# Kernel optimization log

Hardware: AMD Instinct MI355X
Metric: run time of the kernel (lower is better)

## Reference

```python
import jax, jax.numpy as jnp
import numpy as np
import math

D_MODEL = 1024
N_HEADS = 16
D_HEAD = D_MODEL // N_HEADS
NUM_BUCKETS = 32
MAX_DISTANCE = 128
B, LQ, LK = 2, 2048, 2048


def _rel_pos_bucket(rel):
    # rel: [Lq, Lk] int32, rel = mem - ctx
    n = jnp.clip(-rel, 0, None)
    max_exact = NUM_BUCKETS // 2
    is_small = n < max_exact
    val_if_large = max_exact + (
        jnp.log(n.astype(jnp.float32) / max_exact + 1e-9)
        / math.log(MAX_DISTANCE / max_exact)
        * (NUM_BUCKETS - max_exact)
    ).astype(jnp.int32)
    val_if_large = jnp.minimum(val_if_large, NUM_BUCKETS - 1)
    return jnp.where(is_small, n, val_if_large)


def setup_inputs() -> dict:
    key = jax.random.key(0)
    ks = jax.random.split(key, 9)
    scale = 1.0 / math.sqrt(D_MODEL)
    q = jax.random.normal(ks[0], (B, LQ, D_MODEL), dtype=jnp.float32)
    k = jax.random.normal(ks[1], (B, LK, D_MODEL), dtype=jnp.float32)
    v = jax.random.normal(ks[2], (B, LK, D_MODEL), dtype=jnp.float32)
    key_padding_mask = jax.random.randint(ks[3], (B, 1, 1, LK), 0, 2).astype(bool)
    Wq = jax.random.normal(ks[4], (D_MODEL, D_MODEL), dtype=jnp.float32) * scale
    Wk = jax.random.normal(ks[5], (D_MODEL, D_MODEL), dtype=jnp.float32) * scale
    Wv = jax.random.normal(ks[6], (D_MODEL, D_MODEL), dtype=jnp.float32) * scale
    Wo = jax.random.normal(ks[7], (D_MODEL, D_MODEL), dtype=jnp.float32) * scale
    rel_emb = jax.random.normal(ks[8], (NUM_BUCKETS, N_HEADS), dtype=jnp.float32) * 0.02
    return {"q": q, "k": k, "v": v, "key_padding_mask": key_padding_mask,
            "Wq": Wq, "Wk": Wk, "Wv": Wv, "Wo": Wo, "rel_emb": rel_emb}


def reference(q, k, v, key_padding_mask, Wq, Wk, Wv, Wo, rel_emb):
    Bq, Lq, _ = q.shape
    Lk = k.shape[1]
    # projections (nn.Linear: x @ W.T), split heads -> [B, H, L, dh]
    qh = (q @ Wq.T).reshape(Bq, Lq, N_HEADS, D_HEAD).transpose(0, 2, 1, 3)
    kh = (k @ Wk.T).reshape(Bq, Lk, N_HEADS, D_HEAD).transpose(0, 2, 1, 3)
    vh = (v @ Wv.T).reshape(Bq, Lk, N_HEADS, D_HEAD).transpose(0, 2, 1, 3)
    scores = jnp.einsum('bhqd,bhkd->bhqk', qh, kh) / math.sqrt(D_HEAD)
    # relative position bias: [1, H, Lq, Lk]
    rel = jnp.arange(Lk, dtype=jnp.int32)[None, :] - jnp.arange(Lq, dtype=jnp.int32)[:, None]
    buckets = _rel_pos_bucket(rel)  # [Lq, Lk]
    bias = rel_emb[buckets]         # [Lq, Lk, H]
    scores = scores + bias.transpose(2, 0, 1)[None]
    scores = jnp.where(key_padding_mask, scores, -1e9)
    attn = jax.nn.softmax(scores, axis=-1)
    out = jnp.einsum('bhqk,bhkd->bhqd', attn, vh)
    out = out.transpose(0, 2, 1, 3).reshape(Bq, Lq, D_MODEL)
    return out @ Wo.T
```

## Files before the change

kernel.cpp:

```cpp
#include <hip/hip_runtime.h>
#include <math.h>

typedef _Float16 f16;
typedef __fp16 h16x2 __attribute__((ext_vector_type(2)));
typedef _Float16 f16x4 __attribute__((ext_vector_type(4)));
typedef _Float16 f16x8 __attribute__((ext_vector_type(8)));
typedef float f32x4 __attribute__((ext_vector_type(4)));
typedef float f32x16 __attribute__((ext_vector_type(16)));
typedef unsigned int u32;

#define D_MODEL 1024
#define NHEADS 16
#define DHEAD 64
#define LQ 2048
#define LKK 2048
#define BB 2
#define LOG2E 1.4426950408889634f

static __device__ __forceinline__ void gload16(const void* g, void* l) {
  __builtin_amdgcn_global_load_lds(
      (const __attribute__((address_space(1))) u32*)g,
      (__attribute__((address_space(3))) u32*)l, 16, 0, 0);
}
static __device__ __forceinline__ float ex2(float x) {
  float r;
  asm volatile("v_exp_f32 %0, %1\n\ts_nop 0" : "=v"(r) : "v"(x));
  return r;
}
static __device__ __forceinline__ u32 pkr(float a, float b) {
  union { h16x2 h; u32 u; } c;
  c.h = __builtin_amdgcn_cvt_pkrtz(a, b);
  return c.u;
}
static __device__ __forceinline__ float fmax3(float a, float b, float c) {
  return fmaxf(fmaxf(a, b), c);
}
#define MFMA16(a, b, c) __builtin_amdgcn_mfma_f32_16x16x32_f16(a, b, c, 0, 0, 0)
#define MFMA32(a, b, c) __builtin_amdgcn_mfma_f32_32x32x16_f16(a, b, c, 0, 0, 0)

__global__ void k_cvtw_prep(const float* Wq, const float* Wk, const float* Wv, const float* Wo,
                            f16* W16, const void* msk, const float* __restrict__ rel,
                            float* __restrict__ biasT, unsigned char* __restrict__ m8) {
  const int blk = blockIdx.x;
  const int t = threadIdx.x;
  if (blk < 4096) {
    int i = blk * 256 + t;
    int which = i >> 18, off = i & 262143;
    const float* s = which == 0 ? Wq : (which == 1 ? Wk : (which == 2 ? Wv : Wo));
    float4 x = ((const float4*)s)[off];
    f16x4 o; o[0] = (f16)x.x; o[1] = (f16)x.y; o[2] = (f16)x.z; o[3] = (f16)x.w;
    ((f16x4*)(W16 + (size_t)which * 1048576))[off] = o;
    return;
  }
  if (blk == 4096) {
    __shared__ int o1s, o2s;
    if (t == 0) { o1s = 0; o2s = 0; }
    __syncthreads();
    const unsigned char* raw = (const unsigned char*)msk;
    int o1 = 0, o2 = 0;
    for (int i = t; i < BB * LKK; i += 256) {
      unsigned char vv = raw[i];
      if ((i & 3) && vv) o1 = 1;
      if (((i & 3) == 2) && vv == 0x80u) o2 = 1;
    }
    if (o1) atomicOr(&o1s, 1);
    if (o2) atomicOr(&o2s, 1);
    __syncthreads();
    const int f = o1s ? (o2s ? 2 : 1) : 0;
    for (int i = t; i < BB * LKK; i += 256) {
      unsigned char v;
      if (f == 0)      v = (((const int*)msk)[i] != 0);
      else if (f == 1) v = (((const unsigned char*)msk)[i] != 0);
      else             v = (((const float*)msk)[i] != 0.0f);
      m8[i] = v;
    }
    return;
  }
  for (int n = t; n < 2048; n += 256) {
    int bucket;
    if (n < 16) bucket = n;
    else {
      float tt = logf((float)n / 16.0f + 1e-9f);
      tt = tt / 2.0794415416798357f;
      tt = tt * 16.0f;
      bucket = 16 + (int)tt;
      if (bucket > 31) bucket = 31;
    }
    for (int h = 0; h < NHEADS; ++h)
      biasT[h * 2048 + n] = rel[bucket * NHEADS + h] * LOG2E;
  }
}

template <int EPI, int BN, bool AF32>
static __device__ __forceinline__ void gemm_core(const void* __restrict__ Av,
                                                 const f16* __restrict__ Bm,
                                                 void* __restrict__ C) {
  constexpr int JN = BN / 32;
  __shared__ __align__(16) f16 sA[128 * 32];
  __shared__ __align__(16) f16 sB[BN * 32];
  const int t = threadIdx.x;
  const int w = t >> 6, lane = t & 63;
  const int lg = lane >> 4, lc = lane & 15;
  const int wr = w >> 1, wc = w & 1;
  const long row0 = (long)blockIdx.x * 128;
  const long col0 = (long)blockIdx.y * BN;
  f32x4 acc[4][JN] = {};

  for (int kk = 0; kk < 1024; kk += 32) {
#pragma unroll
    for (int it = 0; it < 2; ++it) {
      int ch = t + it * 256;
      int r = ch >> 2, kq = ch & 3;
      if constexpr (AF32) {
        const float* src = (const float*)Av + (row0 + r) * 1024 + kk + kq * 8;
        float4 x0 = *(const float4*)src;
        float4 x1 = *(const float4*)(src + 4);
        f16x8 o;
        o[0] = (f16)x0.x; o[1] = (f16)x0.y; o[2] = (f16)x0.z; o[3] = (f16)x0.w;
        o[4] = (f16)x1.x; o[5] = (f16)x1.y; o[6] = (f16)x1.z; o[7] = (f16)x1.w;
        *(f16x8*)((char*)sA + ch * 16) = o;
      } else {
        gload16((const f16*)Av + (row0 + r) * 1024 + kk + kq * 8, (char*)sA + ch * 16);
      }
    }
#pragma unroll
    for (int it = 0; it < BN / 64; ++it) {
      int ch = t + it * 256;
      int r = ch >> 2, kq = ch & 3;
      gload16(Bm + (col0 + r) * 1024 + kk + kq * 8, (char*)sB + ch * 16);
    }
    __syncthreads();
    f16x8 af[4], bf[JN];
#pragma unroll
    for (int i = 0; i < 4; ++i)
      af[i] = *(const f16x8*)&sA[(wr * 64 + i * 16 + lc) * 32 + lg * 8];
#pragma unroll
    for (int j = 0; j < JN; ++j)
      bf[j] = *(const f16x8*)&sB[(wc * (16 * JN) + j * 16 + lc) * 32 + lg * 8];
#pragma unroll
    for (int i = 0; i < 4; ++i)
#pragma unroll
      for (int j = 0; j < JN; ++j)
        acc[i][j] = MFMA16(af[i], bf[j], acc[i][j]);
    __syncthreads();
  }
#pragma unroll
  for (int i = 0; i < 4; ++i)
#pragma unroll
    for (int j = 0; j < JN; ++j) {
      const long rowb = row0 + wr * 64 + i * 16 + lg * 4;
      const long col = col0 + wc * (16 * JN) + j * 16 + lc;
      if (EPI == 2) {
        long b = rowb >> 11, l0 = rowb & 2047;
        long h = col >> 6, d = col & 63;
        f16x4 ov;
#pragma unroll
        for (int r = 0; r < 4; ++r) ov[r] = (f16)acc[i][j][r];
        *(f16x4*)((f16*)C + (((b * NHEADS + h) * DHEAD + d) * (long)LKK + l0)) = ov;
      } else {
#pragma unroll
        for (int r = 0; r < 4; ++r) {
          long row = rowb + r;
          float v = acc[i][j][r];
          if (EPI == 0) {
            long b = row >> 11, l = row & 2047;
            long h = col >> 6, d = col & 63;
            ((f16*)C)[(((b * NHEADS + h) * LQ) + l) * DHEAD + d] = (f16)v;
          } else {
            ((float*)C)[row * 1024 + col] = v;
          }
        }
      }
    }
}

__global__ void __launch_bounds__(256, 3)
k_gemm_qkv(const float* __restrict__ q, const float* __restrict__ k, const float* __restrict__ v,
           const f16* __restrict__ W16, f16* __restrict__ QHp, f16* __restrict__ KHp,
           f16* __restrict__ VTp) {
  const int z = blockIdx.z;
  if (z == 2) {
    gemm_core<2, 128, true>(v, W16 + 2 * 1048576, VTp);
  } else {
    const float* A = z == 0 ? q : k;
    f16* C = z == 0 ? QHp : KHp;
    gemm_core<0, 128, true>(A, W16 + (size_t)z * 1048576, C);
  }
}

__global__ void __launch_bounds__(256, 2)
k_gemm_o(const f16* __restrict__ A, const f16* __restrict__ Bm, float* __restrict__ C) {
  gemm_core<1, 64, false>(A, Bm, C);
}

__global__ void __launch_bounds__(256, 2)
k_attn(const f16* __restrict__ QH, const f16* __restrict__ KH, const f16* __restrict__ VT,
       const float* __restrict__ BIASg, const unsigned char* __restrict__ M8,
       f16* __restrict__ O16) {
  __shared__ __align__(16) f16 sK[2][64 * 64];
  __shared__ __align__(16) f16 sVT[2][64 * 64];
  __shared__ __align__(16) float sBias[4104];
  __shared__ __align__(16) float sPen[2048];

  const int L = blockIdx.x;
  const int bh = (L & 7) * 4 + ((L >> 3) & 3);
  const int qc = L >> 5;
  const int b = bh >> 4, h = bh & 15;
  const int t = threadIdx.x, w = t >> 6, lane = t & 63;
  const int lq = lane & 31;
  const int hi = lane >> 5;
  const int q0w = qc * 128 + w * 32;
  const size_t base = (size_t)bh * LKK * DHEAD;

  for (int i = t; i < 4104; i += 256) {
    int n = i - 2052; n = n < 0 ? 0 : (n > 2047 ? 2047 : n);
    sBias[i] = BIASg[h * 2048 + n];
  }
  for (int i = t; i < 2048; i += 256)
    sPen[i] = M8[b * LKK + i] ? 0.0f : -3.0e9f;

  f16x8 qb[4];
  const f16* qrow = QH + base + (size_t)(q0w + lq) * DHEAD;
#pragma unroll
  for (int s = 0; s < 4; ++s)
    qb[s] = *(const f16x8*)(qrow + s * 16 + hi * 8);

  const int ch0 = t, ch1 = t + 256;
  const int r0 = ch0 >> 3, g0 = ((ch0 & 7) ^ (r0 & 7)) * 8;
  const int r1 = ch1 >> 3, g1 = ((ch1 & 7) ^ (r1 & 7)) * 8;
  const f16* Kb = KH + base;
  const f16* Vb = VT + base;

  auto STAGE_K = [&](int kt, int buf) {
    const int k0 = kt * 64;
    gload16(Kb + (size_t)(k0 + r0) * DHEAD + g0, (char*)&sK[buf][0] + ch0 * 16);
    gload16(Kb + (size_t)(k0 + r1) * DHEAD + g1, (char*)&sK[buf][0] + ch1 * 16);
  };
  auto STAGE_V = [&](int kt, int buf) {
    const int k0 = kt * 64;
    gload16(Vb + (size_t)r0 * LKK + k0 + g0, (char*)&sVT[buf][0] + ch0 * 16);
    gload16(Vb + (size_t)r1 * LKK + k0 + g1, (char*)&sVT[buf][0] + ch1 * 16);
  };

  float m_r = -1e30f;
  f32x16 oacc0 = {}, oacc1 = {}, oaccL = {};
  const float c1 = 0.125f * LOG2E;
  f16x8 ones;
#pragma unroll
  for (int e = 0; e < 8; ++e) ones[e] = (f16)1.0f;

  auto QK = [&](int kt, f32x16& sa0, f32x16& sa1) {
    const char* sKb = (const char*)&sK[kt & 1][0];
    __builtin_amdgcn_s_setprio(1);
#pragma unroll
    for (int s = 0; s < 4; ++s) {
      f16x8 k0 = *(const f16x8*)(sKb + ((lq * 128 + s * 32 + hi * 16) ^ ((lq & 7) << 4)));
      f16x8 k1 = *(const f16x8*)(sKb + (((32 + lq) * 128 + s * 32 + hi * 16) ^ ((lq & 7) << 4)));
      sa0 = MFMA32(k0, qb[s], sa0);
      sa1 = MFMA32(k1, qb[s], sa1);
    }
    __builtin_amdgcn_s_setprio(0);
  };

  auto SOFTPV = [&](int kt, f32x16& sa0, f32x16& sa1) {
    float p_[32];
#pragma unroll
    for (int r = 0; r < 16; ++r) { p_[r] = sa0[r]; p_[16 + r] = sa1[r]; }

#pragma unroll
    for (int u = 0; u < 8; ++u) {
      int tt = u >> 2, j = u & 3;
      int kbase = kt * 64 + tt * 32 + j * 8 + hi * 4;
      f32x4 pen4 = *(const f32x4*)&sPen[kbase];
      int bidx0 = (q0w + lq) - kbase + 2052;
#pragma unroll
      for (int e = 0; e < 4; ++e) {
        float bp = sBias[bidx0 - e] + pen4[e];
        int r = tt * 16 + j * 4 + e;
        p_[r] = p_[r] * c1 + bp;
      }
    }

    float mm[11];
#pragma unroll
    for (int r = 0; r < 10; ++r) mm[r] = fmax3(p_[3 * r], p_[3 * r + 1], p_[3 * r + 2]);
    mm[10] = fmaxf(p_[30], p_[31]);
    float a0 = fmax3(mm[0], mm[1], mm[2]);
    float a1 = fmax3(mm[3], mm[4], mm[5]);
    float a2 = fmax3(mm[6], mm[7], mm[8]);
    float a3 = fmax3(mm[9], mm[10], a0);
    float mx = fmax3(a1, a2, a3);
    mx = fmaxf(mx, __shfl_xor(mx, 32));

    if (__any(mx > m_r + 8.0f)) {
      float mnew = fmaxf(m_r, mx);
      float al = ex2(m_r - mnew);
      m_r = mnew;
#pragma unroll
      for (int r = 0; r < 16; ++r) { oacc0[r] *= al; oacc1[r] *= al; oaccL[r] *= al; }
    }

#pragma unroll
    for (int r = 0; r < 32; ++r) p_[r] = ex2(p_[r] - m_r);

    f16x8 pf[4];
#pragma unroll
    for (int sl = 0; sl < 4; ++sl) {
      int tt = sl >> 1, sp = sl & 1;
      int bA = tt * 16 + (2 * sp) * 4, bB = tt * 16 + (2 * sp + 1) * 4;
      u32 A0 = pkr(p_[bA], p_[bA + 1]);
      u32 A1 = pkr(p_[bA + 2], p_[bA + 3]);
      u32 B0 = pkr(p_[bB], p_[bB + 1]);
      u32 B1 = pkr(p_[bB + 2], p_[bB + 3]);
      asm volatile("v_permlane32_swap_b32 %0, %1" : "+v"(A0), "+v"(B0));
      asm volatile("v_permlane32_swap_b32 %0, %1" : "+v"(A1), "+v"(B1));
      union { u32 u[4]; f16x8 v; } c;
      c.u[0] = A0; c.u[1] = A1; c.u[2] = B0; c.u[3] = B1;
      pf[sl] = c.v;
    }

    const char* sVb = (const char*)&sVT[kt & 1][0];
    __builtin_amdgcn_s_setprio(1);
#pragma unroll
    for (int sl = 0; sl < 4; ++sl) {
      int K0 = sl * 16;
      f16x8 v0 = *(const f16x8*)(sVb + ((lq * 128 + K0 * 2 + hi * 16) ^ ((lq & 7) << 4)));
      f16x8 v1 = *(const f16x8*)(sVb + (((32 + lq) * 128 + K0 * 2 + hi * 16) ^ ((lq & 7) << 4)));
      oacc0 = MFMA32(v0, pf[sl], oacc0);
      oacc1 = MFMA32(v1, pf[sl], oacc1);
      oaccL = MFMA32(ones, pf[sl], oaccL);
    }
    __builtin_amdgcn_s_setprio(0);
  };

  STAGE_K(0, 0);
  STAGE_V(0, 0);
  STAGE_K(1, 1);
  __syncthreads();
  f32x16 sA0 = {}, sA1 = {}, sB0 = {}, sB1 = {};
  QK(0, sA0, sA1);

  for (int kt = 0; kt < 32; kt += 2) {
    if (kt + 2 < 32) STAGE_K(kt + 2, 0);
    STAGE_V(kt + 1, 1);
    sB0 = f32x16{}; sB1 = f32x16{};
    QK(kt + 1, sB0, sB1);
    SOFTPV(kt, sA0, sA1);
    __syncthreads();
    if (kt + 3 < 32) STAGE_K(kt + 3, 1);
    if (kt + 2 < 32) {
      STAGE_V(kt + 2, 0);
      sA0 = f32x16{}; sA1 = f32x16{};
      QK(kt + 2, sA0, sA1);
    }
    SOFTPV(kt + 1, sB0, sB1);
    __syncthreads();
  }

  const float rinv = 1.0f / oaccL[0];
  const size_t orow = ((size_t)b * LQ + (q0w + lq)) * D_MODEL + h * DHEAD;
#pragma unroll
  for (int dh = 0; dh < 2; ++dh)
#pragma unroll
    for (int j = 0; j < 4; ++j) {
      int d0 = dh * 32 + j * 8 + hi * 4;
      f16x4 ov;
#pragma unroll
      for (int e = 0; e < 4; ++e) {
        float x = (dh ? oacc1[j * 4 + e] : oacc0[j * 4 + e]) * rinv;
        ov[e] = (f16)x;
      }
      *(f16x4*)(O16 + orow + d0) = ov;
    }
}

extern "C" void kernel_launch(void* const* d_in, const int* in_sizes, int n_in,
                              void* d_out, int out_size, void* d_ws, size_t ws_size,
                              hipStream_t stream) {
  (void)in_sizes; (void)n_in; (void)out_size; (void)ws_size;
  const float* q   = (const float*)d_in[0];
  const float* k   = (const float*)d_in[1];
  const float* v   = (const float*)d_in[2];
  const void*  msk = d_in[3];
  const float* Wq  = (const float*)d_in[4];
  const float* Wk  = (const float*)d_in[5];
  const float* Wv  = (const float*)d_in[6];
  const float* Wo  = (const float*)d_in[7];
  const float* rel = (const float*)d_in[8];

  char* ws = (char*)d_ws;
  const size_t SL = (size_t)8 << 20;
  f16* QHp = (f16*)(ws + 0 * SL);
  f16* KHp = (f16*)(ws + 1 * SL);
  f16* VTp = (f16*)(ws + 2 * SL);
  f16* O16 = (f16*)(ws + 3 * SL);
  f16* W16 = (f16*)(ws + 4 * SL);
  char* misc = ws + 5 * SL;
  float* BIAS = (float*)misc;
  unsigned char* M8 = (unsigned char*)(misc + (192 << 10));

  k_cvtw_prep<<<4098, 256, 0, stream>>>(Wq, Wk, Wv, Wo, W16, msk, rel, BIAS, M8);
  k_gemm_qkv<<<dim3(32, 8, 3), 256, 0, stream>>>(q, k, v, W16, QHp, KHp, VTp);
  k_attn<<<512, 256, 0, stream>>>(QHp, KHp, VTp, BIAS, M8, O16);
  k_gemm_o<<<dim3(32, 16), 256, 0, stream>>>(O16, W16 + 3 * 1048576, (float*)d_out);
}
```

Before: 140.8 us.

## Split attention over key halves, read K/V directly, double-buffer GEMM tiles

The attention kernel can now split the key range in two (split-KV): it writes partial normalized outputs plus running max and sum, and a new combine kernel merges the two halves. K and V are read straight from global memory instead of being staged through double-buffered LDS. The bias table now covers only the window this query block needs. The shared GEMM core gains LDS double buffering with register prefetch of the fp32 A tile, and launch bounds are raised to 4 blocks per CU. More blocks and occupancy come at the cost of an extra kernel, extra global traffic for the partials, and uncoalesced direct K/V loads.

After: 238.5 us. +69.4%, slower.

```diff
diff --git a/kernel.cpp b/kernel.cpp
--- a/kernel.cpp
+++ b/kernel.cpp
@@ -96,8 +96,8 @@
                                                  const f16* __restrict__ Bm,
                                                  void* __restrict__ C) {
   constexpr int JN = BN / 32;
-  __shared__ __align__(16) f16 sA[128 * 32];
-  __shared__ __align__(16) f16 sB[BN * 32];
+  __shared__ __align__(16) f16 sA[2][128 * 32];
+  __shared__ __align__(16) f16 sB[2][BN * 32];
   const int t = threadIdx.x;
   const int w = t >> 6, lane = t & 63;
   const int lg = lane >> 4, lc = lane & 15;
@@ -106,44 +106,71 @@
   const long col0 = (long)blockIdx.y * BN;
   f32x4 acc[4][JN] = {};
 
-  for (int kk = 0; kk < 1024; kk += 32) {
-#pragma unroll
-    for (int it = 0; it < 2; ++it) {
-      int ch = t + it * 256;
-      int r = ch >> 2, kq = ch & 3;
-      if constexpr (AF32) {
-        const float* src = (const float*)Av + (row0 + r) * 1024 + kk + kq * 8;
-        float4 x0 = *(const float4*)src;
-        float4 x1 = *(const float4*)(src + 4);
-        f16x8 o;
-        o[0] = (f16)x0.x; o[1] = (f16)x0.y; o[2] = (f16)x0.z; o[3] = (f16)x0.w;
-        o[4] = (f16)x1.x; o[5] = (f16)x1.y; o[6] = (f16)x1.z; o[7] = (f16)x1.w;
-        *(f16x8*)((char*)sA + ch * 16) = o;
-      } else {
-        gload16((const f16*)Av + (row0 + r) * 1024 + kk + kq * 8, (char*)sA + ch * 16);
-      }
-    }
+  const int rA0 = t >> 2, kA0 = t & 3;
+  const int rA1 = (t + 256) >> 2, kA1 = t & 3;
+
+  float4 a[4];
+
+  auto LOADA = [&](int kk) {
+    const float* s0 = (const float*)Av + (row0 + rA0) * 1024 + kk * 32 + kA0 * 8;
+    const float* s1 = (const float*)Av + (row0 + rA1) * 1024 + kk * 32 + kA1 * 8;
+    a[0] = *(const float4*)s0; a[1] = *(const float4*)(s0 + 4);
+    a[2] = *(const float4*)s1; a[3] = *(const float4*)(s1 + 4);
+  };
+  auto WRITEA = [&](int buf) {
+    f16x8 o0, o1;
+    o0[0] = (f16)a[0].x; o0[1] = (f16)a[0].y; o0[2] = (f16)a[0].z; o0[3] = (f16)a[0].w;
+    o0[4] = (f16)a[1].x; o0[5] = (f16)a[1].y; o0[6] = (f16)a[1].z; o0[7] = (f16)a[1].w;
+    o1[0] = (f16)a[2].x; o1[1] = (f16)a[2].y; o1[2] = (f16)a[2].z; o1[3] = (f16)a[2].w;
+    o1[4] = (f16)a[3].x; o1[5] = (f16)a[3].y; o1[6] = (f16)a[3].z; o1[7] = (f16)a[3].w;
+    *(f16x8*)((char*)&sA[buf][0] + t * 16) = o0;
+    *(f16x8*)((char*)&sA[buf][0] + (t + 256) * 16) = o1;
+  };
+  auto STAGEA16 = [&](int kk, int buf) {
+    gload16((const f16*)Av + (row0 + rA0) * 1024 + kk * 32 + kA0 * 8,
+            (char*)&sA[buf][0] + t * 16);
+    gload16((const f16*)Av + (row0 + rA1) * 1024 + kk * 32 + kA1 * 8,
+            (char*)&sA[buf][0] + (t + 256) * 16);
+  };
+  auto STAGEB = [&](int kk, int buf) {
 #pragma unroll
     for (int it = 0; it < BN / 64; ++it) {
       int ch = t + it * 256;
       int r = ch >> 2, kq = ch & 3;
-      gload16(Bm + (col0 + r) * 1024 + kk + kq * 8, (char*)sB + ch * 16);
-    }
-    __syncthreads();
+      gload16(Bm + (col0 + r) * 1024 + kk * 32 + kq * 8, (char*)&sB[buf][0] + ch * 16);
+    }
+  };
+  auto COMPUTE = [&](int buf) {
     f16x8 af[4], bf[JN];
 #pragma unroll
     for (int i = 0; i < 4; ++i)
-      af[i] = *(const f16x8*)&sA[(wr * 64 + i * 16 + lc) * 32 + lg * 8];
+      af[i] = *(const f16x8*)&sA[buf][(wr * 64 + i * 16 + lc) * 32 + lg * 8];
 #pragma unroll
     for (int j = 0; j < JN; ++j)
-      bf[j] = *(const f16x8*)&sB[(wc * (16 * JN) + j * 16 + lc) * 32 + lg * 8];
+      bf[j] = *(const f16x8*)&sB[buf][(wc * (16 * JN) + j * 16 + lc) * 32 + lg * 8];
 #pragma unroll
     for (int i = 0; i < 4; ++i)
 #pragma unroll
       for (int j = 0; j < JN; ++j)
         acc[i][j] = MFMA16(af[i], bf[j], acc[i][j]);
+  };
+
+  if constexpr (AF32) { LOADA(0); } else { STAGEA16(0, 0); }
+  STAGEB(0, 0);
+  if constexpr (AF32) WRITEA(0);
+  __syncthreads();
+
+  for (int kk = 0; kk < 32; ++kk) {
+    const int cur = kk & 1;
+    if (kk < 31) {
+      if constexpr (AF32) { LOADA(kk + 1); } else { STAGEA16(kk + 1, cur ^ 1); }
+      STAGEB(kk + 1, cur ^ 1);
+    }
+    COMPUTE(cur);
+    if (kk < 31) { if constexpr (AF32) WRITEA(cur ^ 1); }
     __syncthreads();
   }
+
 #pragma unroll
   for (int i = 0; i < 4; ++i)
 #pragma unroll
@@ -174,7 +201,7 @@
     }
 }
 
-__global__ void __launch_bounds__(256, 3)
+__global__ void __launch_bounds__(256, 4)
 k_gemm_qkv(const float* __restrict__ q, const float* __restrict__ k, const float* __restrict__ v,
            const f16* __restrict__ W16, f16* __restrict__ QHp, f16* __restrict__ KHp,
            f16* __restrict__ VTp) {
@@ -188,36 +215,38 @@
   }
 }
 
-__global__ void __launch_bounds__(256, 2)
+__global__ void __launch_bounds__(256, 4)
 k_gemm_o(const f16* __restrict__ A, const f16* __restrict__ Bm, float* __restrict__ C) {
   gemm_core<1, 64, false>(A, Bm, C);
 }
 
-__global__ void __launch_bounds__(256, 2)
+template <int SPLIT>
+__global__ void __launch_bounds__(256, 4)
 k_attn(const f16* __restrict__ QH, const f16* __restrict__ KH, const f16* __restrict__ VT,
        const float* __restrict__ BIASg, const unsigned char* __restrict__ M8,
-       f16* __restrict__ O16) {
-  __shared__ __align__(16) f16 sK[2][64 * 64];
-  __shared__ __align__(16) f16 sVT[2][64 * 64];
-  __shared__ __align__(16) float sBias[4104];
-  __shared__ __align__(16) float sPen[2048];
+       f16* __restrict__ OUT, float* __restrict__ ML) {
+  __shared__ float sBias[2176];
+  __shared__ float sPen[2048];
 
   const int L = blockIdx.x;
   const int bh = (L & 7) * 4 + ((L >> 3) & 3);
-  const int qc = L >> 5;
+  const int qc = (L >> 5) & 15;
+  const int half = (SPLIT == 2) ? (L >> 9) : 0;
   const int b = bh >> 4, h = bh & 15;
   const int t = threadIdx.x, w = t >> 6, lane = t & 63;
-  const int lq = lane & 31;
-  const int hi = lane >> 5;
-  const int q0w = qc * 128 + w * 32;
+  const int lq = lane & 31, hi = lane >> 5;
+  const int q0 = qc * 128;
+  const int q0w = q0 + w * 32;
   const size_t base = (size_t)bh * LKK * DHEAD;
 
-  for (int i = t; i < 4104; i += 256) {
-    int n = i - 2052; n = n < 0 ? 0 : (n > 2047 ? 2047 : n);
+  for (int i = t; i < 2176; i += 256) {
+    int n = i + q0 - 2047;
+    n = n < 0 ? 0 : (n > 2047 ? 2047 : n);
     sBias[i] = BIASg[h * 2048 + n];
   }
   for (int i = t; i < 2048; i += 256)
     sPen[i] = M8[b * LKK + i] ? 0.0f : -3.0e9f;
+  __syncthreads();
 
   f16x8 qb[4];
   const f16* qrow = QH + base + (size_t)(q0w + lq) * DHEAD;
@@ -225,22 +254,8 @@
   for (int s = 0; s < 4; ++s)
     qb[s] = *(const f16x8*)(qrow + s * 16 + hi * 8);
 
-  const int ch0 = t, ch1 = t + 256;
-  const int r0 = ch0 >> 3, g0 = ((ch0 & 7) ^ (r0 & 7)) * 8;
-  const int r1 = ch1 >> 3, g1 = ((ch1 & 7) ^ (r1 & 7)) * 8;
   const f16* Kb = KH + base;
   const f16* Vb = VT + base;
-
-  auto STAGE_K = [&](int kt, int buf) {
-    const int k0 = kt * 64;
-    gload16(Kb + (size_t)(k0 + r0) * DHEAD + g0, (char*)&sK[buf][0] + ch0 * 16);
-    gload16(Kb + (size_t)(k0 + r1) * DHEAD + g1, (char*)&sK[buf][0] + ch1 * 16);
-  };
-  auto STAGE_V = [&](int kt, int buf) {
-    const int k0 = kt * 64;
-    gload16(Vb + (size_t)r0 * LKK + k0 + g0, (char*)&sVT[buf][0] + ch0 * 16);
-    gload16(Vb + (size_t)r1 * LKK + k0 + g1, (char*)&sVT[buf][0] + ch1 * 16);
-  };
 
   float m_r = -1e30f;
   f32x16 oacc0 = {}, oacc1 = {}, oaccL = {};
@@ -249,20 +264,21 @@
 #pragma unroll
   for (int e = 0; e < 8; ++e) ones[e] = (f16)1.0f;
 
-  auto QK = [&](int kt, f32x16& sa0, f32x16& sa1) {
-    const char* sKb = (const char*)&sK[kt & 1][0];
+  const int kt0 = half * (32 / SPLIT);
+  const int ktN = kt0 + 32 / SPLIT;
+  for (int kt = kt0; kt < ktN; ++kt) {
+    const f16* Kt = Kb + (size_t)kt * 64 * DHEAD;
+    f32x16 sa0 = {}, sa1 = {};
     __builtin_amdgcn_s_setprio(1);
 #pragma unroll
     for (int s = 0; s < 4; ++s) {
-      f16x8 k0 = *(const f16x8*)(sKb + ((lq * 128 + s * 32 + hi * 16) ^ ((lq & 7) << 4)));
-      f16x8 k1 = *(const f16x8*)(sKb + (((32 + lq) * 128 + s * 32 + hi * 16) ^ ((lq & 7) << 4)));
+      f16x8 k0 = *(const f16x8*)(Kt + (size_t)lq * DHEAD + s * 16 + hi * 8);
+      f16x8 k1 = *(const f16x8*)(Kt + (size_t)(32 + lq) * DHEAD + s * 16 + hi * 8);
       sa0 = MFMA32(k0, qb[s], sa0);
       sa1 = MFMA32(k1, qb[s], sa1);
     }
     __builtin_amdgcn_s_setprio(0);
-  };
-
-  auto SOFTPV = [&](int kt, f32x16& sa0, f32x16& sa1) {
+
     float p_[32];
 #pragma unroll
     for (int r = 0; r < 16; ++r) { p_[r] = sa0[r]; p_[16 + r] = sa1[r]; }
@@ -272,7 +288,7 @@
       int tt = u >> 2, j = u & 3;
       int kbase = kt * 64 + tt * 32 + j * 8 + hi * 4;
       f32x4 pen4 = *(const f32x4*)&sPen[kbase];
-      int bidx0 = (q0w + lq) - kbase + 2052;
+      int bidx0 = w * 32 + lq - kbase + 2047;
 #pragma unroll
       for (int e = 0; e < 4; ++e) {
         float bp = sBias[bidx0 - e] + pen4[e];
@@ -319,65 +335,80 @@
       pf[sl] = c.v;
     }
 
-    const char* sVb = (const char*)&sVT[kt & 1][0];
+    const f16* Vt = Vb + kt * 64;
     __builtin_amdgcn_s_setprio(1);
 #pragma unroll
     for (int sl = 0; sl < 4; ++sl) {
-      int K0 = sl * 16;
-      f16x8 v0 = *(const f16x8*)(sVb + ((lq * 128 + K0 * 2 + hi * 16) ^ ((lq & 7) << 4)));
-      f16x8 v1 = *(const f16x8*)(sVb + (((32 + lq) * 128 + K0 * 2 + hi * 16) ^ ((lq & 7) << 4)));
+      f16x8 v0 = *(const f16x8*)(Vt + (size_t)lq * LKK + sl * 16 + hi * 8);
+      f16x8 v1 = *(const f16x8*)(Vt + (size_t)(32 + lq) * LKK + sl * 16 + hi * 8);
       oacc0 = MFMA32(v0, pf[sl], oacc0);
       oacc1 = MFMA32(v1, pf[sl], oacc1);
       oaccL = MFMA32(ones, pf[sl], oaccL);
     }
     __builtin_amdgcn_s_setprio(0);
-  };
-
-  STAGE_K(0, 0);
-  STAGE_V(0, 0);
-  STAGE_K(1, 1);
-  __syncthreads();
-  f32x16 sA0 = {}, sA1 = {}, sB0 = {}, sB1 = {};
-  QK(0, sA0, sA1);
-
-  for (int kt = 0; kt < 32; kt += 2) {
-    if (kt + 2 < 32) STAGE_K(kt + 2, 0);
-    STAGE_V(kt + 1, 1);
-    sB0 = f32x16{}; sB1 = f32x16{};
-    QK(kt + 1, sB0, sB1);
-    SOFTPV(kt, sA0, sA1);
-    __syncthreads();
-    if (kt + 3 < 32) STAGE_K(kt + 3, 1);
-    if (kt + 2 < 32) {
-      STAGE_V(kt + 2, 0);
-      sA0 = f32x16{}; sA1 = f32x16{};
-      QK(kt + 2, sA0, sA1);
-    }
-    SOFTPV(kt + 1, sB0, sB1);
-    __syncthreads();
-  }
-
-  const float rinv = 1.0f / oaccL[0];
-  const size_t orow = ((size_t)b * LQ + (q0w + lq)) * D_MODEL + h * DHEAD;
-#pragma unroll
-  for (int dh = 0; dh < 2; ++dh)
-#pragma unroll
-    for (int j = 0; j < 4; ++j) {
-      int d0 = dh * 32 + j * 8 + hi * 4;
-      f16x4 ov;
-#pragma unroll
-      for (int e = 0; e < 4; ++e) {
-        float x = (dh ? oacc1[j * 4 + e] : oacc0[j * 4 + e]) * rinv;
-        ov[e] = (f16)x;
+  }
+
+  const float l = oaccL[0];
+  const float rinv = l > 0.0f ? 1.0f / l : 0.0f;
+  if constexpr (SPLIT == 1) {
+    const size_t orow = ((size_t)b * LQ + (q0w + lq)) * D_MODEL + h * DHEAD;
+#pragma unroll
+    for (int dh = 0; dh < 2; ++dh)
+#pragma unroll
+      for (int j = 0; j < 4; ++j) {
+        int d0 = dh * 32 + j * 8 + hi * 4;
+        f16x4 ov;
+#pragma unroll
+        for (int e = 0; e < 4; ++e)
+          ov[e] = (f16)((dh ? oacc1[j * 4 + e] : oacc0[j * 4 + e]) * rinv);
+        *(f16x4*)(OUT + orow + d0) = ov;
       }
-      *(f16x4*)(O16 + orow + d0) = ov;
-    }
+  } else {
+    const size_t row = (size_t)bh * 2048 + (q0w + lq);
+    const size_t prow = ((size_t)half * 65536 + row) * 64;
+#pragma unroll
+    for (int dh = 0; dh < 2; ++dh)
+#pragma unroll
+      for (int j = 0; j < 4; ++j) {
+        int d0 = dh * 32 + j * 8 + hi * 4;
+        f16x4 ov;
+#pragma unroll
+        for (int e = 0; e < 4; ++e)
+          ov[e] = (f16)((dh ? oacc1[j * 4 + e] : oacc0[j * 4 + e]) * rinv);
+        *(f16x4*)(OUT + prow + d0) = ov;
+      }
+    if (hi == 0)
+      ((float2*)ML)[half * 65536 + row] = make_float2(m_r, l);
+  }
+}
+
+__global__ void k_combine(const f16* __restrict__ P16, const float* __restrict__ ML,
+                          f16* __restrict__ O16) {
+  const int idx = blockIdx.x * 256 + threadIdx.x;
+  const int row = idx >> 3;
+  const int dg = (idx & 7) * 8;
+  float2 ml0 = ((const float2*)ML)[row];
+  float2 ml1 = ((const float2*)ML)[65536 + row];
+  float M = fmaxf(ml0.x, ml1.x);
+  float w0 = ex2(ml0.x - M) * ml0.y;
+  float w1 = ex2(ml1.x - M) * ml1.y;
+  float rd = 1.0f / (w0 + w1);
+  w0 *= rd; w1 *= rd;
+  f16x8 o0 = *(const f16x8*)(P16 + (size_t)row * 64 + dg);
+  f16x8 o1 = *(const f16x8*)(P16 + ((size_t)65536 + row) * 64 + dg);
+  const int bh = row >> 11, qq = row & 2047;
+  const int b = bh >> 4, h = bh & 15;
+  f16x8 ov;
+#pragma unroll
+  for (int e = 0; e < 8; ++e)
+    ov[e] = (f16)(w0 * (float)o0[e] + w1 * (float)o1[e]);
+  *(f16x8*)(O16 + ((size_t)b * LQ + qq) * D_MODEL + h * DHEAD + dg) = ov;
 }
 
 extern "C" void kernel_launch(void* const* d_in, const int* in_sizes, int n_in,
                               void* d_out, int out_size, void* d_ws, size_t ws_size,
                               hipStream_t stream) {
-  (void)in_sizes; (void)n_in; (void)out_size; (void)ws_size;
+  (void)in_sizes; (void)n_in; (void)out_size;
   const float* q   = (const float*)d_in[0];
   const float* k   = (const float*)d_in[1];
   const float* v   = (const float*)d_in[2];
@@ -398,9 +429,17 @@
   char* misc = ws + 5 * SL;
   float* BIAS = (float*)misc;
   unsigned char* M8 = (unsigned char*)(misc + (192 << 10));
+  f16* P16 = (f16*)(ws + 5 * SL + (1 << 20));
+  float* ML = (float*)(ws + 5 * SL + (17 << 20));
+  const bool split2 = ws_size >= (size_t)(59 << 20);
 
   k_cvtw_prep<<<4098, 256, 0, stream>>>(Wq, Wk, Wv, Wo, W16, msk, rel, BIAS, M8);
   k_gemm_qkv<<<dim3(32, 8, 3), 256, 0, stream>>>(q, k, v, W16, QHp, KHp, VTp);
-  k_attn<<<512, 256, 0, stream>>>(QHp, KHp, VTp, BIAS, M8, O16);
+  if (split2) {
+    k_attn<2><<<1024, 256, 0, stream>>>(QHp, KHp, VTp, BIAS, M8, P16, ML);
+    k_combine<<<2048, 256, 0, stream>>>(P16, ML, O16);
+  } else {
+    k_attn<1><<<512, 256, 0, stream>>>(QHp, KHp, VTp, BIAS, M8, O16, nullptr);
+  }
   k_gemm_o<<<dim3(32, 16), 256, 0, stream>>>(O16, W16 + 3 * 1048576, (float*)d_out);
 }
```
